# Kernel tuning notes

Measured on AMD Instinct MI355X. Metric: run time of the kernel, lower is better.

## Reference

```python
import jax, jax.numpy as jnp
import numpy as np

K = 16
EPS = 1e-5
NEG_SLOPE = 0.2


def leaky(x):
    return jnp.where(x > 0, x, NEG_SLOPE * x)


def batchnorm_train(x, gamma, beta):
    # x: [B, D]; training-mode BN with biased variance (torch semantics)
    mean = jnp.mean(x, axis=0)
    var = jnp.mean((x - mean) ** 2, axis=0)
    return (x - mean) * jax.lax.rsqrt(var + EPS) * gamma + beta


def setup_inputs() -> dict:
    key = jax.random.key(0)
    ks = jax.random.split(key, 20)
    N, M, D = 30000, 8000, 16
    s = lambda fan_in: 1.0 / np.sqrt(fan_in)
    inp = {
        "xyz": jax.random.normal(ks[0], (N, 3), jnp.float32),
        "atom_xyz": jax.random.normal(ks[1], (M, 3), jnp.float32),
        "atom_types": jax.random.normal(ks[2], (M, D), jnp.float32),
        "Wt1": jax.random.uniform(ks[3], (D, D), jnp.float32, -s(D), s(D)),
        "bt1": jax.random.uniform(ks[4], (D,), jnp.float32, -s(D), s(D)),
        "Wt2": jax.random.uniform(ks[5], (D, D), jnp.float32, -s(D), s(D)),
        "bt2": jax.random.uniform(ks[6], (D,), jnp.float32, -s(D), s(D)),
        "Wt3": jax.random.uniform(ks[7], (D, D), jnp.float32, -s(D), s(D)),
        "bt3": jax.random.uniform(ks[8], (D,), jnp.float32, -s(D), s(D)),
        # embed: conv1 Linear(D+1, D), conv2 Linear(D, D), conv3 Linear(2D, D)
        "W1": jax.random.uniform(ks[9], (D + 1, D), jnp.float32, -s(D + 1), s(D + 1)),
        "b1": jax.random.uniform(ks[10], (D,), jnp.float32, -s(D + 1), s(D + 1)),
        "W2": jax.random.uniform(ks[11], (D, D), jnp.float32, -s(D), s(D)),
        "b2": jax.random.uniform(ks[12], (D,), jnp.float32, -s(D), s(D)),
        "W3": jax.random.uniform(ks[13], (2 * D, D), jnp.float32, -s(2 * D), s(2 * D)),
        "b3": jax.random.uniform(ks[14], (D,), jnp.float32, -s(2 * D), s(2 * D)),
        # batchnorm affine params
        "g1": jnp.ones((D,), jnp.float32),
        "be1": jnp.zeros((D,), jnp.float32),
        "g2": jnp.ones((D,), jnp.float32),
        "be2": jnp.zeros((D,), jnp.float32),
    }
    return inp


def reference(xyz, atom_xyz, atom_types,
              Wt1, bt1, Wt2, bt2, Wt3, bt3,
              W1, b1, W2, b2, W3, b3, g1, be1, g2, be2):
    N, D = xyz.shape[0], atom_types.shape[1]

    # transform_types MLP on atom features: [M, D]
    t = leaky(atom_types @ Wt1 + bt1)
    t = leaky(t @ Wt2 + bt2)
    t = leaky(t @ Wt3 + bt3)

    # kNN: squared distances via GEMM expansion (avoids [N,M,3])
    d2 = (jnp.sum(xyz ** 2, axis=1, keepdims=True)
          + jnp.sum(atom_xyz ** 2, axis=1)[None, :]
          - 2.0 * xyz @ atom_xyz.T)                      # [N, M]
    _, idx = jax.lax.top_k(-d2, K)                       # [N, K] nearest atoms

    # gather neighbor coords, recompute exact squared dists (as in source)
    y_ik = atom_xyz[idx]                                 # [N, K, 3]
    dists = jnp.sum((xyz[:, None, :] - y_ik) ** 2, axis=-1)  # [N, K]

    feat = jnp.concatenate([t[idx], (1.0 / dists)[..., None]], axis=-1)  # [N,K,D+1]

    # conv1 -> leaky -> bn1 -> sum-pool
    fx = feat @ W1 + b1                                  # [N, K, D]
    fx = batchnorm_train(leaky(fx).reshape(-1, D), g1, be1).reshape(N, K, D)
    fx1 = fx.sum(axis=1)                                 # [N, D]

    # conv2 -> leaky -> bn2 -> sum-pool
    fx = fx @ W2 + b2
    fx = batchnorm_train(leaky(fx).reshape(-1, D), g2, be2).reshape(N, K, D)
    fx2 = fx.sum(axis=1)                                 # [N, D]

    return jnp.concatenate([fx1, fx2], axis=-1) @ W3 + b3  # [N, D]
```

## Files before the change

kernel.cpp:

```cpp
#include <hip/hip_runtime.h>

#define N_PTS   30000
#define M_ATOMS 8000
#define D       16
#define KNN     16
#define NGRP    125
#define EPS     1e-5f
#define SLOPE   0.2f
#define BN_COUNT 480000.0f

typedef unsigned long long ull;

__device__ __forceinline__ float leaky(float x) { return x > 0.f ? x : SLOPE * x; }

__device__ __forceinline__ unsigned fkey(float f) {
  unsigned u = __float_as_uint(f);
  return u ^ ((u & 0x80000000u) ? 0xFFFFFFFFu : 0x80000000u);
}

#define DPPSTEP32(v, CTRL) {                                                   \
  unsigned t_ = (unsigned)__builtin_amdgcn_update_dpp(-1, (int)(v), CTRL, 0xF, 0xF, false); \
  (v) = t_ < (v) ? t_ : (v); }

__device__ __forceinline__ unsigned wmin32d(unsigned v) {
  DPPSTEP32(v, 0x111); DPPSTEP32(v, 0x112); DPPSTEP32(v, 0x114);
  DPPSTEP32(v, 0x118); DPPSTEP32(v, 0x142); DPPSTEP32(v, 0x143);
  return (unsigned)__builtin_amdgcn_readlane((int)v, 63);
}

__device__ __forceinline__ void cswap(ull& a, ull& b) {
  ull mn = a < b ? a : b, mx = a < b ? b : a;
  a = mn; b = mx;
}

__device__ __forceinline__ int morton_cell(float x, float y, float z) {
  int cx = min(max((int)floorf((x + 4.f) * 2.f), 0), 15);
  int cy = min(max((int)floorf((y + 4.f) * 2.f), 0), 15);
  int cz = min(max((int)floorf((z + 4.f) * 2.f), 0), 15);
  int c = 0;
#pragma unroll
  for (int b = 0; b < 4; ++b)
    c |= (((cx>>b)&1) << (3*b)) | (((cy>>b)&1) << (3*b+1)) | (((cz>>b)&1) << (3*b+2));
  return c;
}

__global__ void __launch_bounds__(256) kZ_zero(int* __restrict__ bins,
                                               float* __restrict__ gstats) {
  int i = blockIdx.x * 256 + threadIdx.x;
  if (i < 4096) bins[i] = 0;
  else if (i - 4096 < 288) gstats[i - 4096] = 0.f;
}

#define LAYER(IN, OUT, W, B)                                        \
  _Pragma("unroll") for (int j = 0; j < 16; ++j) {                  \
    float acc = B[j];                                               \
    _Pragma("unroll") for (int i = 0; i < 16; ++i)                  \
      acc = fmaf(IN[i], W[i*16+j], acc);                            \
    OUT[j] = leaky(acc);                                            \
  }

__global__ void __launch_bounds__(256) kA_mlp_hist(
    const float* __restrict__ atom_xyz, const float* __restrict__ atom_types,
    const float* __restrict__ Wt1, const float* __restrict__ bt1,
    const float* __restrict__ Wt2, const float* __restrict__ bt2,
    const float* __restrict__ Wt3, const float* __restrict__ bt3,
    const float* __restrict__ W1, const float* __restrict__ b1,
    float* __restrict__ tu_out, int* __restrict__ bins) {
  __shared__ float w1[256], w2[256], w3[256], wc[256];
  __shared__ float bb1[16], bb2[16], bb3[16], bbc[16];
  int tid = threadIdx.x;
  w1[tid] = Wt1[tid]; w2[tid] = Wt2[tid]; w3[tid] = Wt3[tid]; wc[tid] = W1[tid];
  if (tid < 16) { bb1[tid] = bt1[tid]; bb2[tid] = bt2[tid];
                  bb3[tid] = bt3[tid]; bbc[tid] = b1[tid]; }
  __syncthreads();
  int m = blockIdx.x * 256 + tid;
  if (m >= M_ATOMS) return;

  int c = morton_cell(atom_xyz[m*3], atom_xyz[m*3+1], atom_xyz[m*3+2]);
  atomicAdd(&bins[c], 1);

  float u[16], v[16];
  const float4* tp = (const float4*)(atom_types + (size_t)m*16);
  float4 q0 = tp[0], q1 = tp[1], q2 = tp[2], q3 = tp[3];
  u[0]=q0.x; u[1]=q0.y; u[2]=q0.z; u[3]=q0.w;
  u[4]=q1.x; u[5]=q1.y; u[6]=q1.z; u[7]=q1.w;
  u[8]=q2.x; u[9]=q2.y; u[10]=q2.z; u[11]=q2.w;
  u[12]=q3.x; u[13]=q3.y; u[14]=q3.z; u[15]=q3.w;
  LAYER(u, v, w1, bb1);
  LAYER(v, u, w2, bb2);
  LAYER(u, v, w3, bb3);
  float up[16];
#pragma unroll
  for (int j = 0; j < 16; ++j) {
    float acc = bbc[j];
#pragma unroll
    for (int i = 0; i < 16; ++i) acc = fmaf(v[i], wc[i*16+j], acc);
    up[j] = acc;
  }
  float4* op = (float4*)(tu_out + (size_t)m*16);
  op[0] = make_float4(up[0], up[1], up[2], up[3]);
  op[1] = make_float4(up[4], up[5], up[6], up[7]);
  op[2] = make_float4(up[8], up[9], up[10], up[11]);
  op[3] = make_float4(up[12], up[13], up[14], up[15]);
}

__global__ void __launch_bounds__(1024) kB_scan(
    const int* __restrict__ bins, int* __restrict__ cursors) {
  __shared__ int h0[4096], h1[4096];
  int tid = threadIdx.x;
  for (int i = tid; i < 4096; i += 1024) h0[i] = bins[i];
  __syncthreads();
  int* src = h0; int* dst = h1;
  for (int off = 1; off < 4096; off <<= 1) {
    for (int i = tid; i < 4096; i += 1024) {
      int v = src[i];
      if (i >= off) v += src[i-off];
      dst[i] = v;
    }
    __syncthreads();
    int* t = src; src = dst; dst = t;
  }
  for (int i = tid; i < 4096; i += 1024) cursors[i] = i ? src[i-1] : 0;
}

__global__ void __launch_bounds__(256) kC_scatter(
    const float* __restrict__ atom_xyz, int* __restrict__ cursors,
    float4* __restrict__ atoms4s, int* __restrict__ origid) {
  int m = blockIdx.x * 256 + threadIdx.x;
  if (m >= M_ATOMS) return;
  float x = atom_xyz[m*3], y = atom_xyz[m*3+1], z = atom_xyz[m*3+2];
  int c = morton_cell(x, y, z);
  int pos = atomicAdd(&cursors[c], 1);
  atoms4s[pos] = make_float4(x, y, z, fmaf(x,x, fmaf(y,y, z*z)));
  origid[pos] = m;
}

__global__ void __launch_bounds__(256) k_bounds(
    const float4* __restrict__ atoms4s, float4* __restrict__ bounds) {
  int lane = threadIdx.x & 63;
  int g = blockIdx.x * 4 + (threadIdx.x >> 6);
  if (g >= NGRP) return;
  float4 a = atoms4s[(g << 6) + lane];
  float mnx=a.x, mny=a.y, mnz=a.z, mxx=a.x, mxy=a.y, mxz=a.z;
#pragma unroll
  for (int off = 32; off; off >>= 1) {
    mnx = fminf(mnx, __shfl_xor(mnx, off, 64));
    mny = fminf(mny, __shfl_xor(mny, off, 64));
    mnz = fminf(mnz, __shfl_xor(mnz, off, 64));
    mxx = fmaxf(mxx, __shfl_xor(mxx, off, 64));
    mxy = fmaxf(mxy, __shfl_xor(mxy, off, 64));
    mxz = fmaxf(mxz, __shfl_xor(mxz, off, 64));
  }
  if (lane == 0) {
    bounds[2*g]   = make_float4(mnx, mny, mnz, 0.f);
    bounds[2*g+1] = make_float4(mxx, mxy, mxz, 0.f);
  }
}

__global__ void __launch_bounds__(256) k2_knn(
    const float* __restrict__ xyz, const float4* __restrict__ atoms4s,
    const int* __restrict__ origid, const float4* __restrict__ bounds,
    const float* __restrict__ atom_xyz, const float* __restrict__ tu,
    const float* __restrict__ W1,
    int2* __restrict__ pairs, float* __restrict__ gstats) {
  __shared__ float sbuf[4*16*20];
  int tid = threadIdx.x;
  int lane = tid & 63;
  int wid = tid >> 6;
  int n = blockIdx.x * 4 + wid;

  float px = xyz[n*3+0], py = xyz[n*3+1], pz = xyz[n*3+2];
  float x2 = fmaf(px,px, fmaf(py,py, pz*pz));

  unsigned ea, eb = 0xFFFFFFFFu;
  {
    int g = lane;
    float4 mn = bounds[2*g], mx = bounds[2*g+1];
    float dx = fmaxf(fmaxf(mn.x - px, px - mx.x), 0.f);
    float dy = fmaxf(fmaxf(mn.y - py, py - mx.y), 0.f);
    float dz = fmaxf(fmaxf(mn.z - pz, pz - mx.z), 0.f);
    float lb = fmaf(dx,dx, fmaf(dy,dy, dz*dz)) * 0.999f - 1e-4f;
    ea = (fkey(lb) & 0xFFFFFF00u) | (unsigned)g;
  }
  if (lane + 64 < NGRP) {
    int g = lane + 64;
    float4 mn = bounds[2*g], mx = bounds[2*g+1];
    float dx = fmaxf(fmaxf(mn.x - px, px - mx.x), 0.f);
    float dy = fmaxf(fmaxf(mn.y - py, py - mx.y), 0.f);
    float dz = fmaxf(fmaxf(mn.z - pz, pz - mx.z), 0.f);
    float lb = fmaf(dx,dx, fmaf(dy,dy, dz*dz)) * 0.999f - 1e-4f;
    eb = (fkey(lb) & 0xFFFFFF00u) | (unsigned)g;
  }
  unsigned cur = ea < eb ? ea : eb;
  unsigned bak = ea < eb ? eb : ea;

  int gs[4];
#pragma unroll
  for (int r = 0; r < 4; ++r) {
    unsigned m = wmin32d(cur);
    bool own = (cur == m);
    cur = own ? bak : cur;
    bak = own ? 0xFFFFFFFFu : bak;
    gs[r] = (int)(m & 0xFFu);
  }

  float4 A[4]; int OI[4];
#pragma unroll
  for (int r = 0; r < 4; ++r) {
    int base = gs[r] << 6;
    A[r]  = atoms4s[base + lane];
    OI[r] = origid [base + lane];
  }
  ull E[4];
#pragma unroll
  for (int r = 0; r < 4; ++r) {
    float dotp = fmaf(px,A[r].x, fmaf(py,A[r].y, pz*A[r].z));
    float d2 = (x2 + A[r].w) - 2.f*dotp;
    E[r] = ((ull)fkey(d2) << 32) | (unsigned)OI[r];
  }
  cswap(E[0],E[1]); cswap(E[2],E[3]); cswap(E[0],E[2]);
  cswap(E[1],E[3]); cswap(E[1],E[2]);
  unsigned cf0 = (unsigned)(E[0] >> 32), ci0 = (unsigned)E[0];
  unsigned cf1 = (unsigned)(E[1] >> 32), ci1 = (unsigned)E[1];
  unsigned cf2 = (unsigned)(E[2] >> 32), ci2 = (unsigned)E[2];
  unsigned cf3 = (unsigned)(E[3] >> 32), ci3 = (unsigned)E[3];

  ull res = ~0ull;
  unsigned mf = 0, mi = 0;
  for (int r = 0; r < KNN; ++r) {
    mf = wmin32d(cf0);
    ull ball = __ballot(cf0 == mf);
    if (__popcll(ball) == 1) {
      int srcl = (int)(__ffsll(ball) - 1);
      mi = (unsigned)__builtin_amdgcn_readlane((int)ci0, srcl);
    } else {
      unsigned cand = (cf0 == mf) ? ci0 : 0xFFFFFFFFu;
      mi = wmin32d(cand);
    }
    bool own = (cf0 == mf) && (ci0 == mi);
    if (lane == r) res = (((ull)mf) << 32) | mi;
    cf0 = own ? cf1 : cf0; cf1 = own ? cf2 : cf1;
    cf2 = own ? cf3 : cf2; cf3 = own ? 0xFFFFFFFFu : cf3;
    ci0 = own ? ci1 : ci0; ci1 = own ? ci2 : ci1;
    ci2 = own ? ci3 : ci2; ci3 = own ? 0xFFFFFFFFu : ci3;
  }
  ull lv = res;
  ull thresh = (((ull)mf) << 32) | mi;

  for (int it = 0; it < NGRP - 4; ++it) {
    unsigned m = wmin32d(cur);
    if ((m & 0xFFFFFF00u) >= (unsigned)(thresh >> 32)) break;
    bool own = (cur == m);
    cur = own ? bak : cur;
    bak = own ? 0xFFFFFFFFu : bak;
    int base = (int)(m & 0xFFu) << 6;

    float4 a = atoms4s[base + lane];
    int oi2 = origid[base + lane];
    float dotp = fmaf(px,a.x, fmaf(py,a.y, pz*a.z));
    float d2 = (x2 + a.w) - 2.f*dotp;
    ull key = ((ull)fkey(d2) << 32) | (unsigned)oi2;

    ull mk = __ballot(key < thresh);
    while (mk) {
      int src = (int)(__ffsll(mk) - 1);
      mk &= mk - 1;
      unsigned klo = (unsigned)__builtin_amdgcn_readlane((int)(unsigned)key, src);
      unsigned khi = (unsigned)__builtin_amdgcn_readlane((int)(unsigned)(key >> 32), src);
      ull kc = ((ull)khi << 32) | klo;
      if (kc < thresh) {
        bool ins = (lane < KNN) && (kc < lv);
        unsigned pvlo = (unsigned)__builtin_amdgcn_update_dpp(0, (int)(unsigned)lv,        0x111, 0xF, 0xF, false);
        unsigned pvhi = (unsigned)__builtin_amdgcn_update_dpp(0, (int)(unsigned)(lv>>32), 0x111, 0xF, 0xF, false);
        int pins      =           __builtin_amdgcn_update_dpp(0, ins ? 1 : 0,              0x111, 0xF, 0xF, false);
        if (ins) lv = pins ? (((ull)pvhi << 32) | pvlo) : kc;
        unsigned tlo = (unsigned)__builtin_amdgcn_readlane((int)(unsigned)lv, KNN-1);
        unsigned thi = (unsigned)__builtin_amdgcn_readlane((int)(unsigned)(lv >> 32), KNN-1);
        thresh = ((ull)thi << 32) | tlo;
      }
    }
  }

  int oi = (int)(unsigned)(lv & 0xFFFFFFFFull);
  float iv = 0.f;
  if (lane < KNN) {
    float bx = atom_xyz[oi*3+0], by = atom_xyz[oi*3+1], bz = atom_xyz[oi*3+2];
    float dx = px - bx, dy = py - by, dz = pz - bz;
    float dd = fmaf(dx,dx, fmaf(dy,dy, dz*dz));
    iv = 1.f / dd;
    pairs[n*KNN + lane] = make_int2(oi, __float_as_int(iv));

    const float4* up4 = (const float4*)(tu + (size_t)oi*16);
    float4 u0 = up4[0], u1 = up4[1], u2 = up4[2], u3 = up4[3];
    float4* row = (float4*)&sbuf[(wid*16 + lane)*20];
    float4 w;
    w.x = leaky(fmaf(iv, W1[256+ 0], u0.x)); w.y = leaky(fmaf(iv, W1[256+ 1], u0.y));
    w.z = leaky(fmaf(iv, W1[256+ 2], u0.z)); w.w = leaky(fmaf(iv, W1[256+ 3], u0.w));
    row[0] = w;
    w.x = leaky(fmaf(iv, W1[256+ 4], u1.x)); w.y = leaky(fmaf(iv, W1[256+ 5], u1.y));
    w.z = leaky(fmaf(iv, W1[256+ 6], u1.z)); w.w = leaky(fmaf(iv, W1[256+ 7], u1.w));
    row[1] = w;
    w.x = leaky(fmaf(iv, W1[256+ 8], u2.x)); w.y = leaky(fmaf(iv, W1[256+ 9], u2.y));
    w.z = leaky(fmaf(iv, W1[256+10], u2.z)); w.w = leaky(fmaf(iv, W1[256+11], u2.w));
    row[2] = w;
    w.x = leaky(fmaf(iv, W1[256+12], u3.x)); w.y = leaky(fmaf(iv, W1[256+13], u3.y));
    w.z = leaky(fmaf(iv, W1[256+14], u3.z)); w.w = leaky(fmaf(iv, W1[256+15], u3.w));
    row[3] = w;
  }
  __syncthreads();
  {
    int ch = tid & 15, grp = tid >> 4;
    float S = 0.f, Q = 0.f;
#pragma unroll
    for (int i = 0; i < 4; ++i) {
      float v = sbuf[(grp*4 + i)*20 + ch];
      S += v; Q += v*v;
    }
    __syncthreads();
    sbuf[grp*20 + ch] = S;
    sbuf[400 + grp*20 + ch] = Q;
  }
  __syncthreads();
  if (tid < 32) {
    int ch = tid & 15;
    int off = (tid < 16) ? 0 : 400;
    float s = 0.f;
#pragma unroll
    for (int g = 0; g < 16; ++g) s += sbuf[off + g*20 + ch];
    atomicAdd(&gstats[(blockIdx.x & 7)*32 + tid], s);
  }
}

__device__ __forceinline__ void a1_row(const float* __restrict__ tu, int idx,
                                       float iv, const float* wiv, float* a) {
  const float4* up = (const float4*)(tu + (size_t)idx*16);
  float4 r0 = up[0], r1 = up[1], r2 = up[2], r3 = up[3];
  float u[16];
  u[0]=r0.x; u[1]=r0.y; u[2]=r0.z; u[3]=r0.w;
  u[4]=r1.x; u[5]=r1.y; u[6]=r1.z; u[7]=r1.w;
  u[8]=r2.x; u[9]=r2.y; u[10]=r2.z; u[11]=r2.w;
  u[12]=r3.x; u[13]=r3.y; u[14]=r3.z; u[15]=r3.w;
#pragma unroll
  for (int j = 0; j < 16; ++j) a[j] = leaky(fmaf(iv, wiv[j], u[j]));
}

__global__ void __launch_bounds__(256, 4) k4_main(
    const int2* __restrict__ pairs, const float* __restrict__ tu,
    const float* __restrict__ W1,
    const float* __restrict__ W2, const float* __restrict__ b2,
    const float* __restrict__ g1, const float* __restrict__ be1,
    float* __restrict__ fx1_out, float* __restrict__ s2_out,
    float* __restrict__ gstats) {
  __shared__ float wiv[16], w2s[256], b2s[16];
  __shared__ float sc1[16], sh1[16];
  __shared__ float buf[16*16*17];
  int tid = threadIdx.x;
  w2s[tid] = W2[tid];
  if (tid < 16) { wiv[tid] = W1[256 + tid]; b2s[tid] = b2[tid]; }
  if (tid < 16) {
    float s1 = 0.f, q1 = 0.f;
#pragma unroll
    for (int c = 0; c < 8; ++c) { s1 += gstats[c*32 + tid]; q1 += gstats[c*32 + 16 + tid]; }
    float mean = s1 * (1.f/BN_COUNT);
    float var  = q1 * (1.f/BN_COUNT) - mean*mean;
    float sC = g1[tid] / sqrtf(var + EPS);
    sc1[tid] = sC;
    sh1[tid] = be1[tid] - mean * sC;
  }
  __syncthreads();

  int g = blockIdx.x * 256 + tid;
  int p = tid >> 4, k = tid & 15;
  int2 pr = pairs[g];
  int idx = pr.x;
  float iv = __int_as_float(pr.y);
  float h[16], a2[16];
  a1_row(tu, idx, iv, wiv, h);
#pragma unroll
  for (int j = 0; j < 16; ++j) h[j] = fmaf(h[j], sc1[j], sh1[j]);
#pragma unroll
  for (int j = 0; j < 16; ++j) {
    float accj = b2s[j];
#pragma unroll
    for (int i = 0; i < 16; ++i) accj = fmaf(h[i], w2s[i*16+j], accj);
    a2[j] = leaky(accj);
  }

  float* myrow = &buf[(p*16 + k)*17];
  int p2 = tid >> 4, j2 = tid & 15;
#pragma unroll
  for (int j = 0; j < 16; ++j) myrow[j] = h[j];
  __syncthreads();
  {
    float s = 0.f;
#pragma unroll
    for (int kk = 0; kk < 16; ++kk) s += buf[(p2*16+kk)*17 + j2];
    fx1_out[(size_t)blockIdx.x*256 + tid] = s;
  }
  __syncthreads();
#pragma unroll
  for (int j = 0; j < 16; ++j) myrow[j] = a2[j];
  __syncthreads();
  float s2v = 0.f;
#pragma unroll
  for (int kk = 0; kk < 16; ++kk) s2v += buf[(p2*16+kk)*17 + j2];
  s2_out[(size_t)blockIdx.x*256 + tid] = s2v;
  __syncthreads();
#pragma unroll
  for (int j = 0; j < 16; ++j) myrow[j] = a2[j]*a2[j];
  __syncthreads();
  float q2v = 0.f;
#pragma unroll
  for (int kk = 0; kk < 16; ++kk) q2v += buf[(p2*16+kk)*17 + j2];
  __syncthreads();
  buf[p2*17 + j2] = s2v;
  buf[289 + p2*17 + j2] = q2v;
  __syncthreads();
  if (tid < 16) {
    float t1 = 0.f, t2 = 0.f;
#pragma unroll
    for (int pp = 0; pp < 16; ++pp) { t1 += buf[pp*17 + tid]; t2 += buf[289 + pp*17 + tid]; }
    atomicAdd(&gstats[256 + tid], t1);
    atomicAdd(&gstats[272 + tid], t2);
  }
}

__global__ void __launch_bounds__(256) k5_final(
    const float* __restrict__ fx1_in, const float* __restrict__ s2_in,
    const float* __restrict__ gstats,
    const float* __restrict__ W3, const float* __restrict__ b3,
    const float* __restrict__ g2, const float* __restrict__ be2,
    float* __restrict__ out) {
  __shared__ float w[512], bb[16], sc2[16], sh2[16];
  int tid = threadIdx.x;
  w[tid] = W3[tid]; w[256+tid] = W3[256+tid];
  if (tid < 16) {
    bb[tid] = b3[tid];
    float mean = gstats[256+tid] * (1.f/BN_COUNT);
    float var  = gstats[272+tid] * (1.f/BN_COUNT) - mean*mean;
    float s = g2[tid] / sqrtf(var + EPS);
    sc2[tid] = s;
    sh2[tid] = be2[tid] - mean * s;
  }
  __syncthreads();
  int n = blockIdx.x * 256 + tid;
  if (n >= N_PTS) return;

  const float4* f1p = (const float4*)(fx1_in + (size_t)n*16);
  const float4* f2p = (const float4*)(s2_in  + (size_t)n*16);
  float4 x0=f1p[0], x1=f1p[1], x2=f1p[2], x3=f1p[3];
  float4 y0=f2p[0], y1=f2p[1], y2=f2p[2], y3=f2p[3];
  float f1[16] = {x0.x,x0.y,x0.z,x0.w, x1.x,x1.y,x1.z,x1.w,
                  x2.x,x2.y,x2.z,x2.w, x3.x,x3.y,x3.z,x3.w};
  float f2[16] = {y0.x,y0.y,y0.z,y0.w, y1.x,y1.y,y1.z,y1.w,
                  y2.x,y2.y,y2.z,y2.w, y3.x,y3.y,y3.z,y3.w};
#pragma unroll
  for (int i = 0; i < 16; ++i) f2[i] = fmaf(sc2[i], f2[i], 16.f * sh2[i]);

  float4* op = (float4*)(out + (size_t)n*16);
  float o[16];
#pragma unroll
  for (int j = 0; j < 16; ++j) {
    float accj = bb[j];
#pragma unroll
    for (int i = 0; i < 16; ++i) accj = fmaf(f1[i], w[i*16+j], accj);
#pragma unroll
    for (int i = 0; i < 16; ++i) accj = fmaf(f2[i], w[(16+i)*16+j], accj);
    o[j] = accj;
  }
  op[0] = make_float4(o[0], o[1], o[2], o[3]);
  op[1] = make_float4(o[4], o[5], o[6], o[7]);
  op[2] = make_float4(o[8], o[9], o[10], o[11]);
  op[3] = make_float4(o[12], o[13], o[14], o[15]);
}

extern "C" void kernel_launch(void* const* d_in, const int* in_sizes, int n_in,
                              void* d_out, int out_size, void* d_ws, size_t ws_size,
                              hipStream_t stream) {
  const float* xyz        = (const float*)d_in[0];
  const float* atom_xyz   = (const float*)d_in[1];
  const float* atom_types = (const float*)d_in[2];
  const float* Wt1 = (const float*)d_in[3];  const float* bt1 = (const float*)d_in[4];
  const float* Wt2 = (const float*)d_in[5];  const float* bt2 = (const float*)d_in[6];
  const float* Wt3 = (const float*)d_in[7];  const float* bt3 = (const float*)d_in[8];
  const float* W1  = (const float*)d_in[9];  const float* b1  = (const float*)d_in[10];
  const float* W2  = (const float*)d_in[11]; const float* b2  = (const float*)d_in[12];
  const float* W3  = (const float*)d_in[13]; const float* b3  = (const float*)d_in[14];
  const float* g1  = (const float*)d_in[15]; const float* be1 = (const float*)d_in[16];
  const float* g2  = (const float*)d_in[17]; const float* be2 = (const float*)d_in[18];
  float* out = (float*)d_out;

  float* ws = (float*)d_ws;
  float*  tu       = ws;
  int2*   pairs    = (int2*)(ws + 128000);
  float*  fx1      = ws + 1088000;
  float*  s2       = ws + 1568000;
  float*  gstats   = ws + 2048000;
  int*    bins     = (int*)(ws + 2048288);
  int*    cursors  = (int*)(ws + 2052384);
  float4* atoms4s  = (float4*)(ws + 1088000);
  int*    origid   = (int*)(ws + 1120000);
  float4* bounds   = (float4*)(ws + 1128000);

  kZ_zero<<<18, 256, 0, stream>>>(bins, gstats);
  kA_mlp_hist<<<32, 256, 0, stream>>>(atom_xyz, atom_types, Wt1, bt1, Wt2, bt2,
                                      Wt3, bt3, W1, b1, tu, bins);
  kB_scan<<<1, 1024, 0, stream>>>(bins, cursors);
  kC_scatter<<<32, 256, 0, stream>>>(atom_xyz, cursors, atoms4s, origid);
  k_bounds<<<32, 256, 0, stream>>>(atoms4s, bounds);
  k2_knn<<<7500, 256, 0, stream>>>(xyz, atoms4s, origid, bounds, atom_xyz,
                                   tu, W1, pairs, gstats);
  k4_main<<<1875, 256, 0, stream>>>(pairs, tu, W1, W2, b2, g1, be1,
                                    fx1, s2, gstats);
  k5_final<<<118, 256, 0, stream>>>(fx1, s2, gstats, W3, b3, g2, be2, out);
}
```

Before: 212.8 us.

## Fold zeroing and bounds into existing kernels, shrink kNN blocks to two waves

Removes the separate zero kernel by moving histogram counting into per-block shared-memory slices that the scan kernel sums, and lets the scan kernel clear gstats and the bounds buffers. Per-group bounding boxes are now built with atomic min/max on ordered-integer keys during the scatter, and a tiny kernel decodes them, replacing the wave-reduction bounds kernel. The kNN kernel moves from four waves per block to two, and its BN partial-stat slots grow from 8 to 16 to spread atomics. The aim is fewer launches and less atomic contention, at the cost of extra global atomics in the scatter and a 32-slice histogram read in the single-block scan.

Measured after the change: 229.1 us. 1.08x slower.

```diff
diff --git a/kernel.cpp b/kernel.cpp
--- a/kernel.cpp
+++ b/kernel.cpp
@@ -17,6 +17,10 @@
   unsigned u = __float_as_uint(f);
   return u ^ ((u & 0x80000000u) ? 0xFFFFFFFFu : 0x80000000u);
 }
+__device__ __forceinline__ float unfkey(unsigned e) {
+  unsigned u = (e & 0x80000000u) ? (e ^ 0x80000000u) : ~e;
+  return __uint_as_float(u);
+}
 
 #define DPPSTEP32(v, CTRL) {                                                   \
   unsigned t_ = (unsigned)__builtin_amdgcn_update_dpp(-1, (int)(v), CTRL, 0xF, 0xF, false); \
@@ -42,13 +46,6 @@
   for (int b = 0; b < 4; ++b)
     c |= (((cx>>b)&1) << (3*b)) | (((cy>>b)&1) << (3*b+1)) | (((cz>>b)&1) << (3*b+2));
   return c;
-}
-
-__global__ void __launch_bounds__(256) kZ_zero(int* __restrict__ bins,
-                                               float* __restrict__ gstats) {
-  int i = blockIdx.x * 256 + threadIdx.x;
-  if (i < 4096) bins[i] = 0;
-  else if (i - 4096 < 288) gstats[i - 4096] = 0.f;
 }
 
 #define LAYER(IN, OUT, W, B)                                        \
@@ -65,50 +62,64 @@
     const float* __restrict__ Wt2, const float* __restrict__ bt2,
     const float* __restrict__ Wt3, const float* __restrict__ bt3,
     const float* __restrict__ W1, const float* __restrict__ b1,
-    float* __restrict__ tu_out, int* __restrict__ bins) {
+    float* __restrict__ tu_out, int* __restrict__ hist) {
   __shared__ float w1[256], w2[256], w3[256], wc[256];
   __shared__ float bb1[16], bb2[16], bb3[16], bbc[16];
+  __shared__ int lh[4096];
   int tid = threadIdx.x;
+  for (int i = tid; i < 4096; i += 256) lh[i] = 0;
   w1[tid] = Wt1[tid]; w2[tid] = Wt2[tid]; w3[tid] = Wt3[tid]; wc[tid] = W1[tid];
   if (tid < 16) { bb1[tid] = bt1[tid]; bb2[tid] = bt2[tid];
                   bb3[tid] = bt3[tid]; bbc[tid] = b1[tid]; }
   __syncthreads();
   int m = blockIdx.x * 256 + tid;
-  if (m >= M_ATOMS) return;
-
-  int c = morton_cell(atom_xyz[m*3], atom_xyz[m*3+1], atom_xyz[m*3+2]);
-  atomicAdd(&bins[c], 1);
-
-  float u[16], v[16];
-  const float4* tp = (const float4*)(atom_types + (size_t)m*16);
-  float4 q0 = tp[0], q1 = tp[1], q2 = tp[2], q3 = tp[3];
-  u[0]=q0.x; u[1]=q0.y; u[2]=q0.z; u[3]=q0.w;
-  u[4]=q1.x; u[5]=q1.y; u[6]=q1.z; u[7]=q1.w;
-  u[8]=q2.x; u[9]=q2.y; u[10]=q2.z; u[11]=q2.w;
-  u[12]=q3.x; u[13]=q3.y; u[14]=q3.z; u[15]=q3.w;
-  LAYER(u, v, w1, bb1);
-  LAYER(v, u, w2, bb2);
-  LAYER(u, v, w3, bb3);
-  float up[16];
-#pragma unroll
-  for (int j = 0; j < 16; ++j) {
-    float acc = bbc[j];
-#pragma unroll
-    for (int i = 0; i < 16; ++i) acc = fmaf(v[i], wc[i*16+j], acc);
-    up[j] = acc;
-  }
-  float4* op = (float4*)(tu_out + (size_t)m*16);
-  op[0] = make_float4(up[0], up[1], up[2], up[3]);
-  op[1] = make_float4(up[4], up[5], up[6], up[7]);
-  op[2] = make_float4(up[8], up[9], up[10], up[11]);
-  op[3] = make_float4(up[12], up[13], up[14], up[15]);
+  if (m < M_ATOMS) {
+    int c = morton_cell(atom_xyz[m*3], atom_xyz[m*3+1], atom_xyz[m*3+2]);
+    atomicAdd(&lh[c], 1);
+
+    float u[16], v[16];
+    const float4* tp = (const float4*)(atom_types + (size_t)m*16);
+    float4 q0 = tp[0], q1 = tp[1], q2 = tp[2], q3 = tp[3];
+    u[0]=q0.x; u[1]=q0.y; u[2]=q0.z; u[3]=q0.w;
+    u[4]=q1.x; u[5]=q1.y; u[6]=q1.z; u[7]=q1.w;
+    u[8]=q2.x; u[9]=q2.y; u[10]=q2.z; u[11]=q2.w;
+    u[12]=q3.x; u[13]=q3.y; u[14]=q3.z; u[15]=q3.w;
+    LAYER(u, v, w1, bb1);
+    LAYER(v, u, w2, bb2);
+    LAYER(u, v, w3, bb3);
+    float up[16];
+#pragma unroll
+    for (int j = 0; j < 16; ++j) {
+      float acc = bbc[j];
+#pragma unroll
+      for (int i = 0; i < 16; ++i) acc = fmaf(v[i], wc[i*16+j], acc);
+      up[j] = acc;
+    }
+    float4* op = (float4*)(tu_out + (size_t)m*16);
+    op[0] = make_float4(up[0], up[1], up[2], up[3]);
+    op[1] = make_float4(up[4], up[5], up[6], up[7]);
+    op[2] = make_float4(up[8], up[9], up[10], up[11]);
+    op[3] = make_float4(up[12], up[13], up[14], up[15]);
+  }
+  __syncthreads();
+  int* slice = hist + (size_t)blockIdx.x * 4096;
+  for (int i = tid; i < 4096; i += 256) slice[i] = lh[i];
 }
 
 __global__ void __launch_bounds__(1024) kB_scan(
-    const int* __restrict__ bins, int* __restrict__ cursors) {
+    const int* __restrict__ hist, int* __restrict__ cursors,
+    float* __restrict__ gstats, unsigned* __restrict__ benc) {
   __shared__ int h0[4096], h1[4096];
   int tid = threadIdx.x;
-  for (int i = tid; i < 4096; i += 1024) h0[i] = bins[i];
+  for (int i = tid; i < 4096; i += 1024) {
+    int s = 0;
+#pragma unroll
+    for (int b = 0; b < 32; ++b) s += hist[b*4096 + i];
+    h0[i] = s;
+  }
+  if (tid < 544) gstats[tid] = 0.f;
+  if (tid < 375) benc[tid] = 0xFFFFFFFFu;
+  if (tid >= 375 && tid < 750) benc[tid] = 0u;
   __syncthreads();
   int* src = h0; int* dst = h1;
   for (int off = 1; off < 4096; off <<= 1) {
@@ -125,7 +136,8 @@
 
 __global__ void __launch_bounds__(256) kC_scatter(
     const float* __restrict__ atom_xyz, int* __restrict__ cursors,
-    float4* __restrict__ atoms4s, int* __restrict__ origid) {
+    float4* __restrict__ atoms4s, int* __restrict__ origid,
+    unsigned* __restrict__ benc) {
   int m = blockIdx.x * 256 + threadIdx.x;
   if (m >= M_ATOMS) return;
   float x = atom_xyz[m*3], y = atom_xyz[m*3+1], z = atom_xyz[m*3+2];
@@ -133,41 +145,33 @@
   int pos = atomicAdd(&cursors[c], 1);
   atoms4s[pos] = make_float4(x, y, z, fmaf(x,x, fmaf(y,y, z*z)));
   origid[pos] = m;
-}
-
-__global__ void __launch_bounds__(256) k_bounds(
-    const float4* __restrict__ atoms4s, float4* __restrict__ bounds) {
-  int lane = threadIdx.x & 63;
-  int g = blockIdx.x * 4 + (threadIdx.x >> 6);
+  int g = pos >> 6;
+  atomicMin(&benc[g],       fkey(x)); atomicMax(&benc[375+g],     fkey(x));
+  atomicMin(&benc[125+g],   fkey(y)); atomicMax(&benc[375+125+g], fkey(y));
+  atomicMin(&benc[250+g],   fkey(z)); atomicMax(&benc[375+250+g], fkey(z));
+}
+
+__global__ void __launch_bounds__(128) k_dec(
+    const unsigned* __restrict__ benc, float4* __restrict__ bounds) {
+  int g = threadIdx.x;
   if (g >= NGRP) return;
-  float4 a = atoms4s[(g << 6) + lane];
-  float mnx=a.x, mny=a.y, mnz=a.z, mxx=a.x, mxy=a.y, mxz=a.z;
-#pragma unroll
-  for (int off = 32; off; off >>= 1) {
-    mnx = fminf(mnx, __shfl_xor(mnx, off, 64));
-    mny = fminf(mny, __shfl_xor(mny, off, 64));
-    mnz = fminf(mnz, __shfl_xor(mnz, off, 64));
-    mxx = fmaxf(mxx, __shfl_xor(mxx, off, 64));
-    mxy = fmaxf(mxy, __shfl_xor(mxy, off, 64));
-    mxz = fmaxf(mxz, __shfl_xor(mxz, off, 64));
-  }
-  if (lane == 0) {
-    bounds[2*g]   = make_float4(mnx, mny, mnz, 0.f);
-    bounds[2*g+1] = make_float4(mxx, mxy, mxz, 0.f);
-  }
-}
-
-__global__ void __launch_bounds__(256) k2_knn(
+  bounds[2*g]   = make_float4(unfkey(benc[g]),     unfkey(benc[125+g]),
+                              unfkey(benc[250+g]), 0.f);
+  bounds[2*g+1] = make_float4(unfkey(benc[375+g]),     unfkey(benc[375+125+g]),
+                              unfkey(benc[375+250+g]), 0.f);
+}
+
+__global__ void __launch_bounds__(128) k2_knn(
     const float* __restrict__ xyz, const float4* __restrict__ atoms4s,
     const int* __restrict__ origid, const float4* __restrict__ bounds,
     const float* __restrict__ atom_xyz, const float* __restrict__ tu,
     const float* __restrict__ W1,
     int2* __restrict__ pairs, float* __restrict__ gstats) {
-  __shared__ float sbuf[4*16*20];
+  __shared__ float sbuf[2*16*20];
   int tid = threadIdx.x;
   int lane = tid & 63;
   int wid = tid >> 6;
-  int n = blockIdx.x * 4 + wid;
+  int n = blockIdx.x * 2 + wid;
 
   float px = xyz[n*3+0], py = xyz[n*3+1], pz = xyz[n*3+2];
   float x2 = fmaf(px,px, fmaf(py,py, pz*pz));
@@ -318,16 +322,16 @@
     }
     __syncthreads();
     sbuf[grp*20 + ch] = S;
-    sbuf[400 + grp*20 + ch] = Q;
+    sbuf[160 + grp*20 + ch] = Q;
   }
   __syncthreads();
   if (tid < 32) {
     int ch = tid & 15;
-    int off = (tid < 16) ? 0 : 400;
+    int off = (tid < 16) ? 0 : 160;
     float s = 0.f;
 #pragma unroll
-    for (int g = 0; g < 16; ++g) s += sbuf[off + g*20 + ch];
-    atomicAdd(&gstats[(blockIdx.x & 7)*32 + tid], s);
+    for (int g = 0; g < 8; ++g) s += sbuf[off + g*20 + ch];
+    atomicAdd(&gstats[(blockIdx.x & 15)*32 + tid], s);
   }
 }
 
@@ -360,7 +364,7 @@
   if (tid < 16) {
     float s1 = 0.f, q1 = 0.f;
 #pragma unroll
-    for (int c = 0; c < 8; ++c) { s1 += gstats[c*32 + tid]; q1 += gstats[c*32 + 16 + tid]; }
+    for (int c = 0; c < 16; ++c) { s1 += gstats[c*32 + tid]; q1 += gstats[c*32 + 16 + tid]; }
     float mean = s1 * (1.f/BN_COUNT);
     float var  = q1 * (1.f/BN_COUNT) - mean*mean;
     float sC = g1[tid] / sqrtf(var + EPS);
@@ -420,8 +424,8 @@
     float t1 = 0.f, t2 = 0.f;
 #pragma unroll
     for (int pp = 0; pp < 16; ++pp) { t1 += buf[pp*17 + tid]; t2 += buf[289 + pp*17 + tid]; }
-    atomicAdd(&gstats[256 + tid], t1);
-    atomicAdd(&gstats[272 + tid], t2);
+    atomicAdd(&gstats[512 + tid], t1);
+    atomicAdd(&gstats[528 + tid], t2);
   }
 }
 
@@ -436,8 +440,8 @@
   w[tid] = W3[tid]; w[256+tid] = W3[256+tid];
   if (tid < 16) {
     bb[tid] = b3[tid];
-    float mean = gstats[256+tid] * (1.f/BN_COUNT);
-    float var  = gstats[272+tid] * (1.f/BN_COUNT) - mean*mean;
+    float mean = gstats[512+tid] * (1.f/BN_COUNT);
+    float var  = gstats[528+tid] * (1.f/BN_COUNT) - mean*mean;
     float s = g2[tid] / sqrtf(var + EPS);
     sc2[tid] = s;
     sh2[tid] = be2[tid] - mean * s;
@@ -491,25 +495,25 @@
   float* out = (float*)d_out;
 
   float* ws = (float*)d_ws;
-  float*  tu       = ws;
-  int2*   pairs    = (int2*)(ws + 128000);
-  float*  fx1      = ws + 1088000;
-  float*  s2       = ws + 1568000;
-  float*  gstats   = ws + 2048000;
-  int*    bins     = (int*)(ws + 2048288);
-  int*    cursors  = (int*)(ws + 2052384);
-  float4* atoms4s  = (float4*)(ws + 1088000);
-  int*    origid   = (int*)(ws + 1120000);
-  float4* bounds   = (float4*)(ws + 1128000);
-
-  kZ_zero<<<18, 256, 0, stream>>>(bins, gstats);
+  float*    tu      = ws;
+  int2*     pairs   = (int2*)(ws + 128000);
+  float*    fx1     = ws + 1088000;
+  float*    s2      = ws + 1568000;
+  float*    gstats  = ws + 2048000;
+  int*      hist    = (int*)(ws + 2048544);
+  int*      cursors = (int*)(ws + 2179616);
+  unsigned* benc    = (unsigned*)(ws + 2183712);
+  float4*   bounds  = (float4*)(ws + 2184464);
+  float4*   atoms4s = (float4*)(ws + 1088000);
+  int*      origid  = (int*)(ws + 1120000);
+
   kA_mlp_hist<<<32, 256, 0, stream>>>(atom_xyz, atom_types, Wt1, bt1, Wt2, bt2,
-                                      Wt3, bt3, W1, b1, tu, bins);
-  kB_scan<<<1, 1024, 0, stream>>>(bins, cursors);
-  kC_scatter<<<32, 256, 0, stream>>>(atom_xyz, cursors, atoms4s, origid);
-  k_bounds<<<32, 256, 0, stream>>>(atoms4s, bounds);
-  k2_knn<<<7500, 256, 0, stream>>>(xyz, atoms4s, origid, bounds, atom_xyz,
-                                   tu, W1, pairs, gstats);
+                                      Wt3, bt3, W1, b1, tu, hist);
+  kB_scan<<<1, 1024, 0, stream>>>(hist, cursors, gstats, benc);
+  kC_scatter<<<32, 256, 0, stream>>>(atom_xyz, cursors, atoms4s, origid, benc);
+  k_dec<<<1, 128, 0, stream>>>(benc, bounds);
+  k2_knn<<<15000, 128, 0, stream>>>(xyz, atoms4s, origid, bounds, atom_xyz,
+                                    tu, W1, pairs, gstats);
   k4_main<<<1875, 256, 0, stream>>>(pairs, tu, W1, W2, b2, g1, be1,
                                     fx1, s2, gstats);
   k5_final<<<118, 256, 0, stream>>>(fx1, s2, gstats, W3, b3, g2, be2, out);
```
